# Performance work log

Measured on AMD Instinct MI355X. Metric: run time of the kernel, lower is better.

Reference implementation:

```python
import jax, jax.numpy as jnp
from jax import lax
import numpy as np
import math

ALPHA = 1000.0
BETA = 100.0
K = 24
INIT_DIM = 64
STAGES = 4
NUM_POINTS = 2048
B = 16
EPS = 1e-5


def embedding_spe(x, out_dim):
    # x: [..., in_dim] -> [..., out_dim] sinusoidal embedding
    in_dim = x.shape[-1]
    feat_dim = math.ceil(out_dim / (in_dim * 2))
    dim_embed = jnp.asarray(ALPHA ** (np.arange(feat_dim) / feat_dim), x.dtype)
    feat_num = feat_dim * 2 * in_dim
    out_idx = np.linspace(0, feat_num - 1, out_dim).astype(np.int64)
    div = BETA * x[..., None] / dim_embed            # [..., in_dim, feat_dim]
    pe = jnp.stack([jnp.sin(div), jnp.cos(div)], -1)  # [..., in_dim, feat_dim, 2]
    pe = pe.reshape(x.shape[:-1] + (feat_num,))       # order matches torch cat(flatten(stack))
    return pe[..., out_idx]


def fps_single(xyz, npoint):
    # xyz: [N,3] -> indices [npoint] (deterministic start at index 0)
    n = xyz.shape[0]

    def body(carry, _):
        dist, farthest = carry
        centroid = xyz[farthest]
        d = jnp.sum((xyz - centroid) ** 2, -1)
        dist = jnp.minimum(dist, d)
        nxt = jnp.argmax(dist).astype(jnp.int32)
        return (dist, nxt), farthest

    init = (jnp.full((n,), 1e10, xyz.dtype), jnp.array(0, jnp.int32))
    _, idx = lax.scan(body, init, None, length=npoint)
    return idx


def knn(k, xyz, new_xyz):
    # xyz [B,N,3], new_xyz [B,S,3] -> [B,S,k] indices of k nearest points
    d = (jnp.sum(new_xyz ** 2, -1, keepdims=True)
         + jnp.sum(xyz ** 2, -1)[:, None, :]
         - 2.0 * jnp.einsum('bsc,bnc->bsn', new_xyz, xyz))
    _, idx = lax.top_k(-d, k)
    return idx


def gather(pts, idx):
    # pts [B,N,C], idx [B,...] -> [B,...,C]
    b = pts.shape[0]
    bi = jnp.arange(b).reshape((b,) + (1,) * (idx.ndim - 1))
    return pts[bi, idx]


def stage(xyz, feat, npoint, out_dim, gamma, beta_p):
    fps_idx = jax.vmap(lambda p: fps_single(p, npoint))(lax.stop_gradient(xyz))
    xyz_s = gather(xyz, fps_idx)    # [B,S,3]
    feat_s = gather(feat, fps_idx)  # [B,S,C]
    idx_knn = knn(K, lax.stop_gradient(xyz), lax.stop_gradient(xyz_s))  # [B,S,K]
    xyz_knn = gather(xyz, idx_knn)    # [B,S,K,3]
    feat_knn = gather(feat, idx_knn)  # [B,S,K,C]
    # normalize by global (unbiased) std, like torch.std over whole tensor
    xyz_c = xyz_knn - xyz_s[:, :, None, :]
    xyz_knn = xyz_c / (jnp.std(xyz_c, ddof=1) + 1e-05)
    feat_c = feat_knn - feat_s[:, :, None, :]
    feat_knn = feat_c / (jnp.std(feat_c, ddof=1) + 1e-05)
    bsz, s, k, c = feat_knn.shape
    feat_knn = jnp.concatenate(
        [feat_knn, jnp.broadcast_to(feat_s[:, :, None, :], (bsz, s, k, c))], -1)  # [B,S,K,2C]
    # SPE aggregation
    pe = embedding_spe(xyz_knn, out_dim)
    w = (feat_knn + pe) * pe
    # neighbor pooling: max + mean over K
    agg = jnp.max(w, -2) + jnp.mean(w, -2)  # [B,S,out_dim]
    # BatchNorm1d (training-mode batch stats, biased var) + exact GELU
    mean = jnp.mean(agg, axis=(0, 1))
    var = jnp.var(agg, axis=(0, 1))
    y = gamma * (agg - mean) / jnp.sqrt(var + EPS) + beta_p
    return xyz_s, jax.nn.gelu(y, approximate=False)


def setup_inputs() -> dict:
    key = jax.random.key(0)
    ks = jax.random.split(key, 2)
    inp = {'xyz': jax.random.normal(ks[0], (B, NUM_POINTS, 3), jnp.float32)}
    dim = INIT_DIM
    for i in range(STAGES):
        dim *= 2
        inp[f'gamma{i}'] = jnp.ones((dim,), jnp.float32)
        inp[f'beta{i}'] = jnp.zeros((dim,), jnp.float32)
    return inp


def reference(xyz, gamma0, beta0, gamma1, beta1, gamma2, beta2, gamma3, beta3):
    gammas = [gamma0, gamma1, gamma2, gamma3]
    betas = [beta0, beta1, beta2, beta3]
    feat = embedding_spe(xyz, INIT_DIM)
    npoint, dim = NUM_POINTS, INIT_DIM
    for i in range(STAGES):
        dim *= 2
        npoint //= 2
        xyz, feat = stage(xyz, feat, npoint, dim, gammas[i], betas[i])
    return jnp.max(feat, -2) + jnp.mean(feat, -2)  # [B, 1024]
```

## Files before the change

kernel.cpp:

```cpp
#include <hip/hip_runtime.h>
#include <math.h>

#pragma clang fp contract(off)

static constexpr int BATCH = 16;
static constexpr int NPTS0 = 2048;
static constexpr int KNN = 24;

static constexpr size_t OFF_STATS = 0;
static constexpr size_t OFF_BN    = 256;
static constexpr size_t OFF_DE    = 32768;
static constexpr size_t OFF_MAP   = 36864;
static constexpr size_t OFF_XYZ1  = 49152;
static constexpr size_t OFF_XYZ2  = OFF_XYZ1 + (size_t)16*1024*3*4;
static constexpr size_t OFF_XYZ3  = OFF_XYZ2 + (size_t)16*512*3*4;
static constexpr size_t OFF_XYZ4  = OFF_XYZ3 + (size_t)16*256*3*4;
static constexpr size_t OFF_FPS0  = OFF_XYZ4 + (size_t)16*128*3*4;
static constexpr size_t OFF_FPS1  = OFF_FPS0 + (size_t)16*1024*4;
static constexpr size_t OFF_FPS2  = OFF_FPS1 + (size_t)16*512*4;
static constexpr size_t OFF_FPS3  = OFF_FPS2 + (size_t)16*256*4;
static constexpr size_t OFF_KNN   = OFF_FPS3 + (size_t)16*128*4;
static constexpr size_t OFF_FEATA = OFF_KNN + (size_t)16*1024*24*4;
static constexpr size_t OFF_FEATB = OFF_FEATA + (size_t)16*2048*64*4;
static constexpr size_t OFF_FEATS = OFF_FEATB + (size_t)16*2048*64*4;
static constexpr size_t OFF_AGG   = OFF_FEATS + (size_t)16*1024*64*4;
static constexpr size_t WS_NEED   = OFF_AGG + (size_t)16*1024*128*4;

__device__ inline uint64_t kmax64(uint64_t a, uint64_t b) { return a > b ? a : b; }

template <int CTRL>
__device__ inline uint64_t dpp_shift64(uint64_t k) {
  int hi = (int)(unsigned)(k >> 32), lo = (int)(unsigned)k;
  int oh = __builtin_amdgcn_update_dpp(hi, hi, CTRL, 0xF, 0xF, false);
  int ol = __builtin_amdgcn_update_dpp(lo, lo, CTRL, 0xF, 0xF, false);
  return ((uint64_t)(unsigned)oh << 32) | (unsigned)ol;
}
__device__ inline uint64_t wave_reduce_max64(uint64_t k) {
  k = kmax64(k, dpp_shift64<0x111>(k));
  k = kmax64(k, dpp_shift64<0x112>(k));
  k = kmax64(k, dpp_shift64<0x114>(k));
  k = kmax64(k, dpp_shift64<0x118>(k));
  k = kmax64(k, dpp_shift64<0x142>(k));
  k = kmax64(k, dpp_shift64<0x143>(k));
  return k;
}

__device__ inline unsigned sortable_f32(float f) {
  unsigned b = __float_as_uint(f);
  unsigned m = (unsigned)((int)b >> 31) | 0x80000000u;
  return b ^ m;
}

__device__ inline unsigned med3u(unsigned a, unsigned b, unsigned c) {
  unsigned r;
  asm("v_med3_u32 %0, %1, %2, %3" : "=v"(r) : "v"(a), "v"(b), "v"(c));
  return r;
}

__device__ inline void ins24(unsigned kk[KNN], unsigned v) {
#pragma unroll
  for (int e = KNN - 1; e >= 1; --e) kk[e] = med3u(kk[e - 1], kk[e], v);
  kk[0] = kk[0] < v ? kk[0] : v;
}

template <int CTRL>
__device__ inline unsigned dpp1(unsigned v) {
  return (unsigned)__builtin_amdgcn_update_dpp((int)v, (int)v, CTRL, 0xF, 0xF, false);
}

struct R5 { uint64_t k; unsigned x, y, z; };

template <int CTRL>
__device__ inline void red5_step(R5& r) {
  unsigned khi = (unsigned)(r.k >> 32), klo = (unsigned)r.k;
  unsigned shi = dpp1<CTRL>(khi), slo = dpp1<CTRL>(klo);
  unsigned sx = dpp1<CTRL>(r.x), sy = dpp1<CTRL>(r.y), sz = dpp1<CTRL>(r.z);
  uint64_t sk = ((uint64_t)shi << 32) | slo;
  if (sk > r.k) { r.k = sk; r.x = sx; r.y = sy; r.z = sz; }
}
__device__ inline void red5_wave(R5& r) {
  red5_step<0x111>(r); red5_step<0x112>(r); red5_step<0x114>(r);
  red5_step<0x118>(r); red5_step<0x142>(r); red5_step<0x143>(r);
}

__global__ void init_tables(float* __restrict__ de, int* __restrict__ mp) {
  const int outs[5] = {64, 128, 256, 512, 1024};
  const int fds[5]  = {11, 22, 43, 86, 171};
  const int deo[5]  = {0, 11, 33, 76, 162};
  const int mpo[5]  = {0, 64, 192, 448, 960};
  const int tid = threadIdx.x;
  for (int c = 0; c < 5; ++c) {
    const int fd = fds[c], out = outs[c];
    for (int j = tid; j < fd; j += blockDim.x)
      de[deo[c] + j] = (float)pow(1000.0, (double)j / (double)fd);
    const double step = (double)(6 * fd - 1) / (double)(out - 1);
    for (int f = tid; f < out; f += blockDim.x)
      mp[mpo[c] + f] = (int)(step * (double)f);
  }
}

__global__ __launch_bounds__(256) void embed_init(const float* __restrict__ xyz,
                                                  float* __restrict__ feat,
                                                  const float* __restrict__ de,
                                                  const int* __restrict__ mp) {
  int g = blockIdx.x * blockDim.x + threadIdx.x;
  if (g >= BATCH * NPTS0 * 64) return;
  int c = g & 63;
  int bn = g >> 6;
  int m = mp[c];
  int sc = m & 1;
  int a = m >> 1;
  int ci = a / 11;
  int j = a - ci * 11;
  float x = xyz[bn * 3 + ci];
  float ang = (100.0f * x) / de[j];
  feat[g] = sc ? cosf(ang) : sinf(ang);
}

template <int PTS>
__device__ void fps_stage(const float* lds_cur, float* lds_next,
                          int* __restrict__ fps_idx, float* __restrict__ xyz_next,
                          uint64_t* red) {
  const int S = PTS * 128;
  const int tid = threadIdx.x;
  __syncthreads();
  float px[PTS], py[PTS], pz[PTS], dist[PTS];
  const unsigned nl = ~(unsigned)tid;
#pragma unroll
  for (int p = 0; p < PTS; ++p) {
    int gi = tid + p * 256;
    px[p] = lds_cur[3 * gi];
    py[p] = lds_cur[3 * gi + 1];
    pz[p] = lds_cur[3 * gi + 2];
    dist[p] = 1e10f;
  }
  unsigned sel = 0;
  if (tid == 0) {
    fps_idx[0] = 0;
    float a = lds_cur[0], b = lds_cur[1], c = lds_cur[2];
    xyz_next[0] = a; xyz_next[1] = b; xyz_next[2] = c;
    lds_next[0] = a; lds_next[1] = b; lds_next[2] = c;
  }
  for (int t = 1; t < S; ++t) {
    float cx = lds_cur[3 * sel], cy = lds_cur[3 * sel + 1], cz = lds_cur[3 * sel + 2];
    uint64_t kb = 0;
#pragma unroll
    for (int p = 0; p < PTS; ++p) {
      float dx = px[p] - cx, dy = py[p] - cy, dz = pz[p] - cz;
      float dd = dx * dx + dy * dy;
      dd = dd + dz * dz;
      float nd = fminf(dist[p], dd);
      dist[p] = nd;
      uint64_t key = ((uint64_t)__float_as_uint(nd) << 32) | (unsigned)(nl - (unsigned)(p * 256));
      kb = kmax64(kb, key);
    }
    kb = wave_reduce_max64(kb);
    if ((tid & 63) == 63) red[(t & 1) * 4 + (tid >> 6)] = kb;
    __syncthreads();
    uint64_t k0 = red[(t & 1) * 4 + 0], k1 = red[(t & 1) * 4 + 1];
    uint64_t k2 = red[(t & 1) * 4 + 2], k3 = red[(t & 1) * 4 + 3];
    uint64_t km = kmax64(kmax64(k0, k1), kmax64(k2, k3));
    sel = ~(unsigned)km;
    if (tid == 0) {
      fps_idx[t] = (int)sel;
      float a = lds_cur[3 * sel], b = lds_cur[3 * sel + 1], c = lds_cur[3 * sel + 2];
      xyz_next[3 * t] = a; xyz_next[3 * t + 1] = b; xyz_next[3 * t + 2] = c;
      lds_next[3 * t] = a; lds_next[3 * t + 1] = b; lds_next[3 * t + 2] = c;
    }
  }
}

template <int PTS>
__device__ void fps_solo(const float* lds_cur, float* lds_next,
                         int* __restrict__ fps_idx, float* __restrict__ xyz_next) {
  const int S = PTS * 32;
  const int lane = threadIdx.x;
  float px[PTS], py[PTS], pz[PTS], dist[PTS];
  unsigned nlo[PTS];
#pragma unroll
  for (int p = 0; p < PTS; ++p) {
    int gi = lane + p * 64;
    px[p] = lds_cur[3 * gi];
    py[p] = lds_cur[3 * gi + 1];
    pz[p] = lds_cur[3 * gi + 2];
    dist[p] = 1e10f;
    nlo[p] = ~(unsigned)gi;
  }
  float cx = lds_cur[0], cy = lds_cur[1], cz = lds_cur[2];
  if (lane == 0) {
    fps_idx[0] = 0;
    xyz_next[0] = cx; xyz_next[1] = cy; xyz_next[2] = cz;
    lds_next[0] = cx; lds_next[1] = cy; lds_next[2] = cz;
  }
  for (int t = 1; t < S; ++t) {
    uint64_t bk = 0;
    unsigned bx = 0, by = 0, bz = 0;
#pragma unroll
    for (int p = 0; p < PTS; ++p) {
      float dx = px[p] - cx, dy = py[p] - cy, dz = pz[p] - cz;
      float dd = dx * dx + dy * dy;
      dd = dd + dz * dz;
      float nd = fminf(dist[p], dd);
      dist[p] = nd;
      uint64_t kp = ((uint64_t)__float_as_uint(nd) << 32) | nlo[p];
      bool w = kp > bk;
      bk = w ? kp : bk;
      bx = w ? __float_as_uint(px[p]) : bx;
      by = w ? __float_as_uint(py[p]) : by;
      bz = w ? __float_as_uint(pz[p]) : bz;
    }
    R5 r; r.k = bk; r.x = bx; r.y = by; r.z = bz;
    red5_wave(r);
    unsigned klo = (unsigned)__builtin_amdgcn_readlane((int)(unsigned)r.k, 63);
    cx = __uint_as_float((unsigned)__builtin_amdgcn_readlane((int)r.x, 63));
    cy = __uint_as_float((unsigned)__builtin_amdgcn_readlane((int)r.y, 63));
    cz = __uint_as_float((unsigned)__builtin_amdgcn_readlane((int)r.z, 63));
    if (lane == 0) {
      fps_idx[t] = (int)(~klo);
      xyz_next[3 * t] = cx; xyz_next[3 * t + 1] = cy; xyz_next[3 * t + 2] = cz;
      lds_next[3 * t] = cx; lds_next[3 * t + 1] = cy; lds_next[3 * t + 2] = cz;
    }
  }
}

__global__ __launch_bounds__(256) void fps_all(const float* __restrict__ xyz0,
                                               float* __restrict__ xyz1, float* __restrict__ xyz2,
                                               float* __restrict__ xyz3, float* __restrict__ xyz4,
                                               int* __restrict__ i0, int* __restrict__ i1,
                                               int* __restrict__ i2, int* __restrict__ i3) {
  __shared__ float lds[3 * (2048 + 1024 + 512 + 256 + 128)];
  __shared__ uint64_t red[8];
  const int b = blockIdx.x;
  float* l0 = lds;
  float* l1 = l0 + 3 * 2048;
  float* l2 = l1 + 3 * 1024;
  float* l3 = l2 + 3 * 512;
  float* l4 = l3 + 3 * 256;
  for (int t = threadIdx.x; t < 3 * 2048; t += 256) l0[t] = xyz0[(size_t)b * 3 * 2048 + t];
  fps_stage<8>(l0, l1, i0 + b * 1024, xyz1 + (size_t)b * 1024 * 3, red);
  __syncthreads();
  if (threadIdx.x >= 64) return;
  fps_solo<16>(l1, l2, i1 + b * 512, xyz2 + (size_t)b * 512 * 3);
  fps_solo<8>(l2, l3, i2 + b * 256, xyz3 + (size_t)b * 256 * 3);
  fps_solo<4>(l3, l4, i3 + b * 128, xyz4 + (size_t)b * 128 * 3);
}

static constexpr int MGS = 29;
__global__ __launch_bounds__(256) void knn_tau(const float* __restrict__ db_xyz,
                                               const float* __restrict__ q_xyz,
                                               unsigned* __restrict__ tau,
                                               int Np, int S) {
  extern __shared__ float smem[];
  float4* db = (float4*)smem;
  unsigned* mg = (unsigned*)(db + Np);
  const int tid = threadIdx.x, lane = tid & 63, wv = tid >> 6;
  const int bpb = S >> 6;
  const int b = blockIdx.x / bpb;
  const int qbase = (blockIdx.x % bpb) * 64;
  for (int j = tid; j < Np; j += 256) {
    float x = db_xyz[((size_t)b * Np + j) * 3 + 0];
    float y = db_xyz[((size_t)b * Np + j) * 3 + 1];
    float z = db_xyz[((size_t)b * Np + j) * 3 + 2];
    float pn = x * x + y * y;
    pn = pn + z * z;
    db[j] = make_float4(x, y, z, pn);
  }
  __syncthreads();
  const int s = qbase + lane;
  float qx = q_xyz[((size_t)b * S + s) * 3 + 0];
  float qy = q_xyz[((size_t)b * S + s) * 3 + 1];
  float qz = q_xyz[((size_t)b * S + s) * 3 + 2];
  float qn = qx * qx + qy * qy;
  qn = qn + qz * qz;
  unsigned kk[KNN];
#pragma unroll
  for (int e = 0; e < KNN; ++e) kk[e] = 0xFFFFFFFFu;
  const int cpw = Np >> 2;
  const int beg = wv * cpw, end = beg + cpw;
  for (int j0 = beg; j0 < end; j0 += 8) {
    float4 p[8];
#pragma unroll
    for (int u = 0; u < 8; ++u) p[u] = db[j0 + u];
#pragma unroll
    for (int u = 0; u < 8; ++u) {
      float dot = fmaf(qz, p[u].z, fmaf(qy, p[u].y, qx * p[u].x));
      float d = (qn + p[u].w) - 2.0f * dot;
      unsigned su = sortable_f32(d);
      if (__any(su < kk[KNN - 1])) ins24(kk, su);
    }
  }
  unsigned* myrow = mg + (wv * 64 + lane) * MGS;
#pragma unroll
  for (int e = 0; e < KNN; ++e) myrow[e] = kk[e];
  __syncthreads();
  if (wv == 0) {
    for (int w = 1; w < 4; ++w) {
      const unsigned* orow = mg + (w * 64 + lane) * MGS;
#pragma unroll
      for (int e = 0; e < KNN; ++e) {
        unsigned v = orow[e];
        if (__any(v < kk[KNN - 1])) ins24(kk, v);
      }
    }
    tau[(size_t)b * S + s] = kk[KNN - 1];
  }
}

__global__ __launch_bounds__(256) void knn_collect(const float* __restrict__ db_xyz,
                                                   const float* __restrict__ q_xyz,
                                                   const unsigned* __restrict__ tau,
                                                   int* __restrict__ out_idx,
                                                   int Np, int S) {
  __shared__ uint64_t bufA[4][24];
  __shared__ uint64_t bufB[4][24];
  const int lane = threadIdx.x & 63, wv = threadIdx.x >> 6;
  const int qi = blockIdx.x * 4 + wv;
  const int b = qi / S, s = qi % S;
  float qx = q_xyz[((size_t)b * S + s) * 3 + 0];
  float qy = q_xyz[((size_t)b * S + s) * 3 + 1];
  float qz = q_xyz[((size_t)b * S + s) * 3 + 2];
  float qn = qx * qx + qy * qy;
  qn = qn + qz * qz;
  const unsigned tt = tau[qi];
  int cntA = 0, cntB = 0;
  const unsigned long long lmlt = (1ull << lane) - 1;
  const int iters = Np >> 6;
  for (int it = 0; it < iters; ++it) {
    int j = it * 64 + lane;
    float x = db_xyz[((size_t)b * Np + j) * 3 + 0];
    float y = db_xyz[((size_t)b * Np + j) * 3 + 1];
    float z = db_xyz[((size_t)b * Np + j) * 3 + 2];
    float pn = x * x + y * y;
    pn = pn + z * z;
    float dot = fmaf(qz, z, fmaf(qy, y, qx * x));
    float d = (qn + pn) - 2.0f * dot;
    unsigned su = sortable_f32(d);
    unsigned long long mlt = __ballot(su < tt);
    unsigned long long meq = __ballot(su == tt);
    if (mlt) {
      int pos = cntA + __popcll(mlt & lmlt);
      if (su < tt && pos < 24) bufA[wv][pos] = ((uint64_t)su << 32) | (unsigned)j;
      cntA += __popcll(mlt);
    }
    if (meq) {
      int pos = cntB + __popcll(meq & lmlt);
      if (su == tt && pos < 24) bufB[wv][pos] = ((uint64_t)su << 32) | (unsigned)j;
      cntB += __popcll(meq);
    }
  }
  uint64_t v = (lane < cntA) ? bufA[wv][lane] : ~0ull;
#pragma unroll
  for (int k = 2; k <= 64; k <<= 1) {
#pragma unroll
    for (int m = k >> 1; m > 0; m >>= 1) {
      uint64_t o = __shfl_xor(v, m);
      bool takemin = (((lane & k) == 0) == ((lane & m) == 0));
      uint64_t mn = v < o ? v : o;
      uint64_t mx = v < o ? o : v;
      v = takemin ? mn : mx;
    }
  }
  if (lane < KNN) {
    uint64_t key = (lane < cntA) ? v : bufB[wv][lane - cntA];
    out_idx[(size_t)qi * KNN + lane] = (int)(unsigned)key;
  }
}

__global__ __launch_bounds__(256) void gather_feat_s(const float* __restrict__ feat,
                                                     const int* __restrict__ fidx,
                                                     float* __restrict__ out, int Np, int S, int C) {
  int g = blockIdx.x * blockDim.x + threadIdx.x;
  if (g >= BATCH * S * C) return;
  int c = g % C;
  int bs = g / C;
  int s = bs % S;
  int b = bs / S;
  int src = fidx[b * S + s];
  out[g] = feat[((size_t)b * Np + src) * C + c];
}

__global__ __launch_bounds__(256) void center_reduce(const float* __restrict__ xyz,
                                                     const float* __restrict__ xyz_s,
                                                     const float* __restrict__ feat,
                                                     const float* __restrict__ feat_s,
                                                     const int* __restrict__ kidx,
                                                     double* __restrict__ sums,
                                                     int Np, int S, int C) {
  int g = blockIdx.x * blockDim.x + threadIdx.x;
  int total = BATCH * S * KNN;
  double sx = 0, sxx = 0, sf = 0, sff = 0;
  if (g < total) {
    int bs = g / KNN;
    int s = bs % S;
    int b = bs / S;
    int j = kidx[g];
    const float* pc = xyz + ((size_t)b * Np + j) * 3;
    const float* qc = xyz_s + ((size_t)b * S + s) * 3;
    for (int c = 0; c < 3; ++c) {
      float v = pc[c] - qc[c];
      sx += (double)v;
      sxx += (double)v * (double)v;
    }
    const float4* fr = (const float4*)(feat + ((size_t)b * Np + j) * C);
    const float4* fs = (const float4*)(feat_s + ((size_t)b * S + s) * C);
    for (int c = 0; c < C / 4; ++c) {
      float4 a = fr[c], bq = fs[c];
      float v0 = a.x - bq.x, v1 = a.y - bq.y, v2 = a.z - bq.z, v3 = a.w - bq.w;
      sf += (double)v0 + (double)v1 + (double)v2 + (double)v3;
      sff += (double)v0 * v0 + (double)v1 * v1 + (double)v2 * v2 + (double)v3 * v3;
    }
  }
#pragma unroll
  for (int m = 1; m < 64; m <<= 1) {
    sx += __shfl_xor(sx, m);
    sxx += __shfl_xor(sxx, m);
    sf += __shfl_xor(sf, m);
    sff += __shfl_xor(sff, m);
  }
  __shared__ double part[4][4];
  int wv = threadIdx.x >> 6;
  if ((threadIdx.x & 63) == 0) { part[wv][0] = sx; part[wv][1] = sxx; part[wv][2] = sf; part[wv][3] = sff; }
  __syncthreads();
  if (threadIdx.x == 0) {
    double a = 0, b2 = 0, c2 = 0, d2 = 0;
    for (int w = 0; w < 4; ++w) { a += part[w][0]; b2 += part[w][1]; c2 += part[w][2]; d2 += part[w][3]; }
    atomicAdd(&sums[0], a);
    atomicAdd(&sums[1], b2);
    atomicAdd(&sums[2], c2);
    atomicAdd(&sums[3], d2);
  }
}

template <int CH>
__global__ __launch_bounds__(256) void agg_kernel(const float* __restrict__ xyz,
                                                  const float* __restrict__ xyz_s,
                                                  const float* __restrict__ feat,
                                                  const float* __restrict__ feat_s,
                                                  const int* __restrict__ kidx,
                                                  const double* __restrict__ csums,
                                                  const float* __restrict__ de,
                                                  const int* __restrict__ mp,
                                                  float* __restrict__ agg,
                                                  int Np, int S, int C, int fd,
                                                  double nx_d, double nf_d) {
  const int lane = threadIdx.x & 63;
  const int wv = threadIdx.x >> 6;
  const int q = blockIdx.x * 4 + wv;
  const int s = q % S;
  const int b = q / S;
  double sxd = csums[0], sxxd = csums[1], sfd = csums[2], sffd = csums[3];
  float stdx = sqrtf((float)((sxxd - sxd * sxd / nx_d) / (nx_d - 1.0)));
  float stdf = sqrtf((float)((sffd - sfd * sfd / nf_d) / (nf_d - 1.0)));
  float invx = 1.0f / (stdx + 1e-5f);
  float invf = 1.0f / (stdf + 1e-5f);
  float cx = xyz_s[((size_t)b * S + s) * 3 + 0];
  float cy = xyz_s[((size_t)b * S + s) * 3 + 1];
  float cz = xyz_s[((size_t)b * S + s) * 3 + 2];
  const float* fsrow = feat_s + ((size_t)b * S + s) * C;
  int ci[CH];
  float dev[CH], fsv[CH];
  bool issin[CH], fh[CH];
#pragma unroll
  for (int ch = 0; ch < CH; ++ch) {
    int f = ch * 64 + lane;
    int m = mp[f];
    issin[ch] = (m & 1) == 0;
    int a = m >> 1;
    int cc = a / fd;
    ci[ch] = cc;
    dev[ch] = de[a - cc * fd];
    fh[ch] = f < C;
    fsv[ch] = fh[ch] ? fsrow[f] : fsrow[f - C];
  }
  float wmax[CH], wsum[CH];
#pragma unroll
  for (int ch = 0; ch < CH; ++ch) { wmax[ch] = -3.4e38f; wsum[ch] = 0.f; }
  const int* krow = kidx + ((size_t)b * S + s) * KNN;
  for (int k = 0; k < KNN; ++k) {
    int j = krow[k];
    const float* pr = xyz + ((size_t)b * Np + j) * 3;
    float n0 = (pr[0] - cx) * invx;
    float n1 = (pr[1] - cy) * invx;
    float n2 = (pr[2] - cz) * invx;
    const float* fr = feat + ((size_t)b * Np + j) * C;
#pragma unroll
    for (int ch = 0; ch < CH; ++ch) {
      float xv = (ci[ch] == 0) ? n0 : ((ci[ch] == 1) ? n1 : n2);
      float ang = (100.0f * xv) / dev[ch];
      float sv, cv;
      sincosf(ang, &sv, &cv);
      float pef = issin[ch] ? sv : cv;
      int f = ch * 64 + lane;
      float val = fh[ch] ? (fr[f] - fsv[ch]) * invf : fsv[ch];
      float w = (val + pef) * pef;
      wmax[ch] = fmaxf(wmax[ch], w);
      wsum[ch] += w;
    }
  }
  float* arow = agg + (size_t)q * (CH * 64);
#pragma unroll
  for (int ch = 0; ch < CH; ++ch) {
    int f = ch * 64 + lane;
    arow[f] = wmax[ch] + wsum[ch] / (float)KNN;
  }
}

__global__ __launch_bounds__(256) void bn_reduce(const float* __restrict__ agg,
                                                 double* __restrict__ bns,
                                                 int R, int D) {
  int r0 = blockIdx.x * 64;
  for (int c = threadIdx.x; c < D; c += 256) {
    double s = 0, ss = 0;
    for (int r = 0; r < 64; ++r) {
      float v = agg[(size_t)(r0 + r) * D + c];
      s += (double)v;
      ss += (double)v * (double)v;
    }
    atomicAdd(&bns[c], s);
    atomicAdd(&bns[D + c], ss);
  }
}

__global__ __launch_bounds__(256) void bn_apply(const float* __restrict__ agg,
                                                const double* __restrict__ bns,
                                                const float* __restrict__ gamma,
                                                const float* __restrict__ beta,
                                                float* __restrict__ outf, int R, int D) {
  int g = blockIdx.x * blockDim.x + threadIdx.x;
  if (g >= R * D) return;
  int c = g % D;
  double n = (double)R;
  double mu = bns[c] / n;
  double var = bns[D + c] / n - mu * mu;
  float mean = (float)mu;
  float rstd = 1.0f / sqrtf((float)var + 1e-5f);
  float x = (agg[g] - mean) * rstd;
  float y = gamma[c] * x + beta[c];
  float e = erff(y * 0.70710678118654752440f);
  outf[g] = 0.5f * y * (1.0f + e);
}

__global__ __launch_bounds__(256) void final_kernel(const float* __restrict__ feat,
                                                    float* __restrict__ out) {
  int g = blockIdx.x * blockDim.x + threadIdx.x;
  if (g >= BATCH * 1024) return;
  int f = g % 1024;
  int b = g / 1024;
  const float* base = feat + (size_t)b * 128 * 1024 + f;
  float mx = -3.4e38f;
  float sm = 0.f;
  for (int s = 0; s < 128; ++s) {
    float v = base[(size_t)s * 1024];
    mx = fmaxf(mx, v);
    sm += v;
  }
  out[g] = mx + sm / 128.0f;
}

extern "C" void kernel_launch(void* const* d_in, const int* in_sizes, int n_in,
                              void* d_out, int out_size, void* d_ws, size_t ws_size,
                              hipStream_t stream) {
  (void)in_sizes; (void)n_in; (void)out_size;
  if (ws_size < WS_NEED) return;
  const float* xyz = (const float*)d_in[0];
  const float* gam[4] = {(const float*)d_in[1], (const float*)d_in[3], (const float*)d_in[5], (const float*)d_in[7]};
  const float* bet[4] = {(const float*)d_in[2], (const float*)d_in[4], (const float*)d_in[6], (const float*)d_in[8]};
  char* ws = (char*)d_ws;
  double* stats = (double*)(ws + OFF_STATS);
  double* bns = (double*)(ws + OFF_BN);
  float* de = (float*)(ws + OFF_DE);
  int* mp = (int*)(ws + OFF_MAP);
  float* xyz1 = (float*)(ws + OFF_XYZ1);
  float* xyz2 = (float*)(ws + OFF_XYZ2);
  float* xyz3 = (float*)(ws + OFF_XYZ3);
  float* xyz4 = (float*)(ws + OFF_XYZ4);
  int* fpsI[4] = {(int*)(ws + OFF_FPS0), (int*)(ws + OFF_FPS1), (int*)(ws + OFF_FPS2), (int*)(ws + OFF_FPS3)};
  int* kidx = (int*)(ws + OFF_KNN);
  float* feata = (float*)(ws + OFF_FEATA);
  float* featb = (float*)(ws + OFF_FEATB);
  float* feats = (float*)(ws + OFF_FEATS);
  unsigned* tau = (unsigned*)(ws + OFF_FEATS);
  float* agg = (float*)(ws + OFF_AGG);

  hipMemsetAsync(ws, 0, 32768, stream);
  init_tables<<<1, 256, 0, stream>>>(de, mp);
  fps_all<<<16, 256, 0, stream>>>(xyz, xyz1, xyz2, xyz3, xyz4, fpsI[0], fpsI[1], fpsI[2], fpsI[3]);
  embed_init<<<(BATCH * NPTS0 * 64) / 256, 256, 0, stream>>>(xyz, feata, de, mp);

  const int Ns[4] = {2048, 1024, 512, 256};
  const int Cs[4] = {64, 128, 256, 512};
  const int fdv[4] = {22, 43, 86, 171};
  const int deo[4] = {11, 33, 76, 162};
  const int mpo[4] = {64, 192, 448, 960};
  const float* xin[5] = {xyz, xyz1, xyz2, xyz3, xyz4};
  float* fcur = feata;
  float* fnext = featb;
  int bnoff = 0;
  for (int i = 0; i < 4; ++i) {
    const int Np = Ns[i], S = Np / 2, C = Cs[i], D = 2 * C;
    size_t tau_lds = (size_t)Np * 16 + (size_t)4 * 64 * MGS * 4;
    knn_tau<<<16 * (S / 64), 256, tau_lds, stream>>>(xin[i], xin[i + 1], tau, Np, S);
    knn_collect<<<(BATCH * S) / 4, 256, 0, stream>>>(xin[i], xin[i + 1], tau, kidx, Np, S);
    gather_feat_s<<<(BATCH * S * C) / 256, 256, 0, stream>>>(fcur, fpsI[i], feats, Np, S, C);
    const int tuples = BATCH * S * KNN;
    center_reduce<<<(tuples + 255) / 256, 256, 0, stream>>>(xin[i], xin[i + 1], fcur, feats, kidx,
                                                            stats + 4 * i, Np, S, C);
    double nx = (double)tuples * 3.0;
    double nf = (double)tuples * (double)C;
    dim3 ag((BATCH * S) / 4);
    switch (D / 64) {
      case 2:
        agg_kernel<2><<<ag, 256, 0, stream>>>(xin[i], xin[i + 1], fcur, feats, kidx, stats + 4 * i,
                                              de + deo[i], mp + mpo[i], agg, Np, S, C, fdv[i], nx, nf);
        break;
      case 4:
        agg_kernel<4><<<ag, 256, 0, stream>>>(xin[i], xin[i + 1], fcur, feats, kidx, stats + 4 * i,
                                              de + deo[i], mp + mpo[i], agg, Np, S, C, fdv[i], nx, nf);
        break;
      case 8:
        agg_kernel<8><<<ag, 256, 0, stream>>>(xin[i], xin[i + 1], fcur, feats, kidx, stats + 4 * i,
                                              de + deo[i], mp + mpo[i], agg, Np, S, C, fdv[i], nx, nf);
        break;
      default:
        agg_kernel<16><<<ag, 256, 0, stream>>>(xin[i], xin[i + 1], fcur, feats, kidx, stats + 4 * i,
                                               de + deo[i], mp + mpo[i], agg, Np, S, C, fdv[i], nx, nf);
        break;
    }
    const int R = BATCH * S;
    bn_reduce<<<R / 64, 256, 0, stream>>>(agg, bns + bnoff, R, D);
    bn_apply<<<(R * D) / 256, 256, 0, stream>>>(agg, bns + bnoff, gam[i], bet[i], fnext, R, D);
    bnoff += 2 * D;
    float* t = fcur; fcur = fnext; fnext = t;
  }
  final_kernel<<<(BATCH * 1024) / 256, 256, 0, stream>>>(fcur, (float*)d_out);
}
```

Before: 1.967 ms.

## Drop gather_feat_s kernel and batch FPS solo-stage global writes

Removes the gather_feat_s kernel and instead reads the sampled-point feature row directly from the full feature tensor via the FPS index inside center_reduce and agg_kernel. This saves one launch and one materialised copy per stage, at the cost of an extra indirect load per tuple. The single-wave FPS stages now buffer their selected indices in LDS and write indices and coordinates to global memory in one coalesced pass after the loop. This takes scalar global stores off the serial per-iteration critical path.

```diff
diff --git a/kernel.cpp b/kernel.cpp
--- a/kernel.cpp
+++ b/kernel.cpp
@@ -22,8 +22,8 @@
 static constexpr size_t OFF_KNN   = OFF_FPS3 + (size_t)16*128*4;
 static constexpr size_t OFF_FEATA = OFF_KNN + (size_t)16*1024*24*4;
 static constexpr size_t OFF_FEATB = OFF_FEATA + (size_t)16*2048*64*4;
-static constexpr size_t OFF_FEATS = OFF_FEATB + (size_t)16*2048*64*4;
-static constexpr size_t OFF_AGG   = OFF_FEATS + (size_t)16*1024*64*4;
+static constexpr size_t OFF_TAU   = OFF_FEATB + (size_t)16*2048*64*4;
+static constexpr size_t OFF_AGG   = OFF_TAU + (size_t)16*1024*64*4;
 static constexpr size_t WS_NEED   = OFF_AGG + (size_t)16*1024*128*4;
 
 __device__ inline uint64_t kmax64(uint64_t a, uint64_t b) { return a > b ? a : b; }
@@ -171,7 +171,7 @@
 }
 
 template <int PTS>
-__device__ void fps_solo(const float* lds_cur, float* lds_next,
+__device__ void fps_solo(const float* lds_cur, float* lds_next, int* idx_buf,
                          int* __restrict__ fps_idx, float* __restrict__ xyz_next) {
   const int S = PTS * 32;
   const int lane = threadIdx.x;
@@ -188,8 +188,7 @@
   }
   float cx = lds_cur[0], cy = lds_cur[1], cz = lds_cur[2];
   if (lane == 0) {
-    fps_idx[0] = 0;
-    xyz_next[0] = cx; xyz_next[1] = cy; xyz_next[2] = cz;
+    idx_buf[0] = 0;
     lds_next[0] = cx; lds_next[1] = cy; lds_next[2] = cz;
   }
   for (int t = 1; t < S; ++t) {
@@ -216,11 +215,12 @@
     cy = __uint_as_float((unsigned)__builtin_amdgcn_readlane((int)r.y, 63));
     cz = __uint_as_float((unsigned)__builtin_amdgcn_readlane((int)r.z, 63));
     if (lane == 0) {
-      fps_idx[t] = (int)(~klo);
-      xyz_next[3 * t] = cx; xyz_next[3 * t + 1] = cy; xyz_next[3 * t + 2] = cz;
+      idx_buf[t] = (int)(~klo);
       lds_next[3 * t] = cx; lds_next[3 * t + 1] = cy; lds_next[3 * t + 2] = cz;
     }
   }
+  for (int u = lane; u < S; u += 64) fps_idx[u] = idx_buf[u];
+  for (int u = lane; u < 3 * S; u += 64) xyz_next[u] = lds_next[u];
 }
 
 __global__ __launch_bounds__(256) void fps_all(const float* __restrict__ xyz0,
@@ -230,6 +230,7 @@
                                                int* __restrict__ i2, int* __restrict__ i3) {
   __shared__ float lds[3 * (2048 + 1024 + 512 + 256 + 128)];
   __shared__ uint64_t red[8];
+  __shared__ int idxb[512 + 256 + 128];
   const int b = blockIdx.x;
   float* l0 = lds;
   float* l1 = l0 + 3 * 2048;
@@ -240,9 +241,9 @@
   fps_stage<8>(l0, l1, i0 + b * 1024, xyz1 + (size_t)b * 1024 * 3, red);
   __syncthreads();
   if (threadIdx.x >= 64) return;
-  fps_solo<16>(l1, l2, i1 + b * 512, xyz2 + (size_t)b * 512 * 3);
-  fps_solo<8>(l2, l3, i2 + b * 256, xyz3 + (size_t)b * 256 * 3);
-  fps_solo<4>(l3, l4, i3 + b * 128, xyz4 + (size_t)b * 128 * 3);
+  fps_solo<16>(l1, l2, idxb, i1 + b * 512, xyz2 + (size_t)b * 512 * 3);
+  fps_solo<8>(l2, l3, idxb + 512, i2 + b * 256, xyz3 + (size_t)b * 256 * 3);
+  fps_solo<4>(l3, l4, idxb + 768, i3 + b * 128, xyz4 + (size_t)b * 128 * 3);
 }
 
 static constexpr int MGS = 29;
@@ -366,23 +367,10 @@
   }
 }
 
-__global__ __launch_bounds__(256) void gather_feat_s(const float* __restrict__ feat,
-                                                     const int* __restrict__ fidx,
-                                                     float* __restrict__ out, int Np, int S, int C) {
-  int g = blockIdx.x * blockDim.x + threadIdx.x;
-  if (g >= BATCH * S * C) return;
-  int c = g % C;
-  int bs = g / C;
-  int s = bs % S;
-  int b = bs / S;
-  int src = fidx[b * S + s];
-  out[g] = feat[((size_t)b * Np + src) * C + c];
-}
-
 __global__ __launch_bounds__(256) void center_reduce(const float* __restrict__ xyz,
                                                      const float* __restrict__ xyz_s,
                                                      const float* __restrict__ feat,
-                                                     const float* __restrict__ feat_s,
+                                                     const int* __restrict__ fidx,
                                                      const int* __restrict__ kidx,
                                                      double* __restrict__ sums,
                                                      int Np, int S, int C) {
@@ -394,6 +382,7 @@
     int s = bs % S;
     int b = bs / S;
     int j = kidx[g];
+    int src = fidx[bs];
     const float* pc = xyz + ((size_t)b * Np + j) * 3;
     const float* qc = xyz_s + ((size_t)b * S + s) * 3;
     for (int c = 0; c < 3; ++c) {
@@ -402,7 +391,7 @@
       sxx += (double)v * (double)v;
     }
     const float4* fr = (const float4*)(feat + ((size_t)b * Np + j) * C);
-    const float4* fs = (const float4*)(feat_s + ((size_t)b * S + s) * C);
+    const float4* fs = (const float4*)(feat + ((size_t)b * Np + src) * C);
     for (int c = 0; c < C / 4; ++c) {
       float4 a = fr[c], bq = fs[c];
       float v0 = a.x - bq.x, v1 = a.y - bq.y, v2 = a.z - bq.z, v3 = a.w - bq.w;
@@ -435,7 +424,7 @@
 __global__ __launch_bounds__(256) void agg_kernel(const float* __restrict__ xyz,
                                                   const float* __restrict__ xyz_s,
                                                   const float* __restrict__ feat,
-                                                  const float* __restrict__ feat_s,
+                                                  const int* __restrict__ fidx,
                                                   const int* __restrict__ kidx,
                                                   const double* __restrict__ csums,
                                                   const float* __restrict__ de,
@@ -456,7 +445,7 @@
   float cx = xyz_s[((size_t)b * S + s) * 3 + 0];
   float cy = xyz_s[((size_t)b * S + s) * 3 + 1];
   float cz = xyz_s[((size_t)b * S + s) * 3 + 2];
-  const float* fsrow = feat_s + ((size_t)b * S + s) * C;
+  const float* fsrow = feat + ((size_t)b * Np + fidx[b * S + s]) * C;
   int ci[CH];
   float dev[CH], fsv[CH];
   bool issin[CH], fh[CH];
@@ -578,8 +567,7 @@
   int* kidx = (int*)(ws + OFF_KNN);
   float* feata = (float*)(ws + OFF_FEATA);
   float* featb = (float*)(ws + OFF_FEATB);
-  float* feats = (float*)(ws + OFF_FEATS);
-  unsigned* tau = (unsigned*)(ws + OFF_FEATS);
+  unsigned* tau = (unsigned*)(ws + OFF_TAU);
   float* agg = (float*)(ws + OFF_AGG);
 
   hipMemsetAsync(ws, 0, 32768, stream);
@@ -601,28 +589,27 @@
     size_t tau_lds = (size_t)Np * 16 + (size_t)4 * 64 * MGS * 4;
     knn_tau<<<16 * (S / 64), 256, tau_lds, stream>>>(xin[i], xin[i + 1], tau, Np, S);
     knn_collect<<<(BATCH * S) / 4, 256, 0, stream>>>(xin[i], xin[i + 1], tau, kidx, Np, S);
-    gather_feat_s<<<(BATCH * S * C) / 256, 256, 0, stream>>>(fcur, fpsI[i], feats, Np, S, C);
     const int tuples = BATCH * S * KNN;
-    center_reduce<<<(tuples + 255) / 256, 256, 0, stream>>>(xin[i], xin[i + 1], fcur, feats, kidx,
+    center_reduce<<<(tuples + 255) / 256, 256, 0, stream>>>(xin[i], xin[i + 1], fcur, fpsI[i], kidx,
                                                             stats + 4 * i, Np, S, C);
     double nx = (double)tuples * 3.0;
     double nf = (double)tuples * (double)C;
     dim3 ag((BATCH * S) / 4);
     switch (D / 64) {
       case 2:
-        agg_kernel<2><<<ag, 256, 0, stream>>>(xin[i], xin[i + 1], fcur, feats, kidx, stats + 4 * i,
+        agg_kernel<2><<<ag, 256, 0, stream>>>(xin[i], xin[i + 1], fcur, fpsI[i], kidx, stats + 4 * i,
                                               de + deo[i], mp + mpo[i], agg, Np, S, C, fdv[i], nx, nf);
         break;
       case 4:
-        agg_kernel<4><<<ag, 256, 0, stream>>>(xin[i], xin[i + 1], fcur, feats, kidx, stats + 4 * i,
+        agg_kernel<4><<<ag, 256, 0, stream>>>(xin[i], xin[i + 1], fcur, fpsI[i], kidx, stats + 4 * i,
                                               de + deo[i], mp + mpo[i], agg, Np, S, C, fdv[i], nx, nf);
         break;
       case 8:
-        agg_kernel<8><<<ag, 256, 0, stream>>>(xin[i], xin[i + 1], fcur, feats, kidx, stats + 4 * i,
+        agg_kernel<8><<<ag, 256, 0, stream>>>(xin[i], xin[i + 1], fcur, fpsI[i], kidx, stats + 4 * i,
                                               de + deo[i], mp + mpo[i], agg, Np, S, C, fdv[i], nx, nf);
         break;
       default:
-        agg_kernel<16><<<ag, 256, 0, stream>>>(xin[i], xin[i + 1], fcur, feats, kidx, stats + 4 * i,
+        agg_kernel<16><<<ag, 256, 0, stream>>>(xin[i], xin[i + 1], fcur, fpsI[i], kidx, stats + 4 * i,
                                                de + deo[i], mp + mpo[i], agg, Np, S, C, fdv[i], nx, nf);
         break;
     }
```

New measurement: 1.919 ms. 2.4% less time.
